# Optimization experiments

Hardware: AMD Instinct MI355X
Metric: run time of the kernel (lower is better)

## Reference

```python
import math
import jax, jax.numpy as jnp
import numpy as np

BH, S, DK = 64, 1024, 64   # batch*heads, seq_len, head dim
FG, FL = 32, 32            # global / local enrichment feature dims
H, B = 16, 4               # mask layout [heads, batch, seq]


def setup_inputs() -> dict:
    key = jax.random.key(0)
    k1, k2, k3, k4, k5, k6 = jax.random.split(key, 6)
    return {
        "query": jax.random.normal(k1, (BH, S, DK), dtype=jnp.float32),
        "key": jax.random.normal(k2, (BH, S, DK), dtype=jnp.float32),
        "value": jax.random.normal(k3, (BH, S, DK), dtype=jnp.float32),
        "local_f": jax.random.normal(k4, (BH, S, FL), dtype=jnp.float32),
        "global_f": jax.random.normal(k5, (BH, S, FG), dtype=jnp.float32),
        "mask": jax.random.randint(k6, (H, B, S), 0, 2, dtype=jnp.int32),
    }


def reference(query, key, value, local_f, global_f, mask):
    dk = query.shape[-1]
    # enrich q/k with global then local features (matches torch concat order)
    pq = jnp.concatenate([query, global_f, local_f], axis=2)   # [BH, S, dk+fg+fl]
    pk = jnp.concatenate([key, global_f, local_f], axis=2)
    scores = jnp.einsum("bqd,bkd->bqk", pq, pk) / math.sqrt(dk)  # [BH, S, S]
    # mask [H, B, S] -> [H*B, S] -> broadcast over query positions
    m = mask.reshape(-1, mask.shape[-1])[:, None, :]            # [H*B, 1, S]
    scores = jnp.where(m == 1, jnp.float32(-1e9), scores)
    attn = jax.nn.softmax(scores, axis=-1)
    return jnp.einsum("bqk,bkd->bqd", attn, value)              # [BH, S, dk]
```

## Files before the change

### kernel.cpp

```cpp
#include <hip/hip_runtime.h>
#include <hip/hip_bf16.h>


#define BHn 64
#define Sn  1024
#define NT  16
#define BK  64
#define BQ  64
#define KSTR 152
#define VSTR 72
#define KTILE (BK*KSTR*2)
#define VTILE (64*VSTR*2)
#define OSTR 68

typedef __attribute__((ext_vector_type(8)))  __bf16 bf16x8;
typedef __attribute__((ext_vector_type(16))) float  f32x16;
typedef __attribute__((ext_vector_type(4)))  unsigned int u32x4;
typedef __attribute__((ext_vector_type(2)))  unsigned int u32x2;

__device__ __forceinline__ unsigned f2bf1(float a){
    union { float f; unsigned u; } c; c.f = a;
    return (c.u + 0x7fffu + ((c.u >> 16) & 1u)) >> 16;
}
__device__ __forceinline__ unsigned f2bf2(float a, float b){
    return f2bf1(a) | (f2bf1(b) << 16);
}
__device__ __forceinline__ void wr4(unsigned short* p, float4 f){
    u32x2 w; w.x = f2bf2(f.x, f.y); w.y = f2bf2(f.z, f.w);
    *(u32x2*)p = w;
}
__device__ __forceinline__ unsigned pkbf(float a, float b){
    return __builtin_amdgcn_perm(__builtin_bit_cast(unsigned, b),
                                 __builtin_bit_cast(unsigned, a), 0x07060302u);
}
__device__ __forceinline__ void gld_lds16(const void* g, void* l){
    __builtin_amdgcn_global_load_lds(
        (const __attribute__((address_space(1))) unsigned int*)g,
        (__attribute__((address_space(3))) unsigned int*)l, 16, 0, 0);
}

__global__ __launch_bounds__(256)
void attn_prep(const float* __restrict__ K, const float* __restrict__ V,
               const float* __restrict__ LF, const float* __restrict__ GF,
               const int* __restrict__ M,
               unsigned short* __restrict__ Kp, unsigned short* __restrict__ Vp)
{
    __shared__ float vlds[64*65];
    const int tid = threadIdx.x;
    const int bh = blockIdx.x >> 4, ti = blockIdx.x & 15;
    const int kb = ti * BK;
    unsigned short* ktg = Kp + (size_t)(bh*NT + ti) * (BK*KSTR);
    unsigned int*   vtg = (unsigned int*)(Vp + (size_t)(bh*NT + ti) * (64*VSTR));

    #pragma unroll
    for (int i=0;i<4;i++){
        int idx = tid + 256*i, k = idx>>4, c = idx&15;
        float4 f = *(const float4*)(V + ((size_t)bh*Sn + kb + k)*64 + c*4);
        vlds[(c*4+0)*65 + k] = f.x;
        vlds[(c*4+1)*65 + k] = f.y;
        vlds[(c*4+2)*65 + k] = f.z;
        vlds[(c*4+3)*65 + k] = f.w;
    }
    #pragma unroll
    for (int i=0;i<4;i++){
        int idx = tid + 256*i, row = idx>>4, c = idx&15;
        float4 f = *(const float4*)(K + ((size_t)bh*Sn + kb + row)*64 + c*4);
        wr4(ktg + row*KSTR + c*4, f);
    }
    #pragma unroll
    for (int i=0;i<2;i++){
        int idx = tid + 256*i, row = idx>>3, c = idx&7;
        float4 f = *(const float4*)(GF + ((size_t)bh*Sn + kb + row)*32 + c*4);
        wr4(ktg + row*KSTR + 64 + c*4, f);
    }
    #pragma unroll
    for (int i=0;i<2;i++){
        int idx = tid + 256*i, row = idx>>3, c = idx&7;
        float4 f = *(const float4*)(LF + ((size_t)bh*Sn + kb + row)*32 + c*4);
        wr4(ktg + row*KSTR + 96 + c*4, f);
    }
    if (tid < BK){
        int mv = M[(size_t)bh*Sn + kb + tid];
        u32x4 w; w[0] = (mv == 1) ? 0x0000ceacu : 0u;
        w[1]=0u; w[2]=0u; w[3]=0u;
        *(u32x4*)(ktg + tid*KSTR + 128) = w;
        u32x4 z; z[0]=0u; z[1]=0u; z[2]=0u; z[3]=0u;
        *(u32x4*)(ktg + tid*KSTR + 136) = z;
        *(u32x4*)(ktg + tid*KSTR + 144) = z;
    }
    __syncthreads();
    #pragma unroll
    for (int i=0;i<8;i++){
        int idx = tid + 256*i, d = idx>>5, j = idx&31;
        vtg[d*36 + j] = f2bf2(vlds[d*65 + 2*j], vlds[d*65 + 2*j + 1]);
    }
}

__global__ __launch_bounds__(256, 4)
void attn_main(const float* __restrict__ Q, const unsigned short* __restrict__ Kp,
               const unsigned short* __restrict__ Vp,
               const float* __restrict__ GF, const float* __restrict__ LF,
               float* __restrict__ O)
{
    __shared__ __align__(16) unsigned char smem[KTILE + VTILE];
    unsigned short* kt_s = (unsigned short*)smem;
    unsigned short* vt_s = (unsigned short*)(smem + KTILE);

    const int tid  = threadIdx.x;
    const int wave = tid >> 6, lane = tid & 63;
    const int l31  = lane & 31, h = lane >> 5;
    const int qh   = wave >> 1;
    const int kp   = wave & 1;
    const int bh = blockIdx.x & 63;
    const int qb = blockIdx.x >> 6;
    const float SCL = 0.18033688011112042f;

    const int qrow = qb*BQ + qh*32 + l31;
    u32x4 qf[9];
    #pragma unroll
    for (int dc = 0; dc < 8; dc++){
        const int cb = dc*16 + 8*h;
        const float* src;
        if (cb < 64)      src = Q  + ((size_t)bh*Sn + qrow)*64 + cb;
        else if (cb < 96) src = GF + ((size_t)bh*Sn + qrow)*32 + (cb - 64);
        else              src = LF + ((size_t)bh*Sn + qrow)*32 + (cb - 96);
        float4 f0 = *(const float4*)src;
        float4 f1 = *(const float4*)(src + 4);
        qf[dc][0] = f2bf2(f0.x*SCL, f0.y*SCL);
        qf[dc][1] = f2bf2(f0.z*SCL, f0.w*SCL);
        qf[dc][2] = f2bf2(f1.x*SCL, f1.y*SCL);
        qf[dc][3] = f2bf2(f1.z*SCL, f1.w*SCL);
    }
    qf[8][0] = h ? 0u : 0x00003f80u;
    qf[8][1] = 0u; qf[8][2] = 0u; qf[8][3] = 0u;

    f32x16 oacc[2];
    #pragma unroll
    for (int dt=0; dt<2; dt++)
        #pragma unroll
        for (int r=0; r<16; r++) oacc[dt][r] = 0.f;
    float lrun = 0.f;

    for (int t = 0; t < NT; t++){
        __syncthreads();
        const unsigned char* gK = (const unsigned char*)Kp + (size_t)(bh*NT + t)*KTILE;
        const unsigned char* gV = (const unsigned char*)Vp + (size_t)(bh*NT + t)*VTILE;
        #pragma unroll
        for (int i=0;i<7;i++){
            int c = wave*7 + i;
            if (c < 19) gld_lds16(gK + (size_t)c*1024 + lane*16, smem + c*1024);
            else        gld_lds16(gV + (size_t)(c-19)*1024 + lane*16,
                                  smem + KTILE + (size_t)(c-19)*1024);
        }
        __syncthreads();

        f32x16 acc;
        #pragma unroll
        for (int r=0;r<16;r++) acc[r] = 0.f;
        #pragma unroll
        for (int dc=0; dc<9; dc++){
            u32x4 ar = *(const u32x4*)(kt_s + (kp*32 + l31)*KSTR + dc*16 + 8*h);
            acc = __builtin_amdgcn_mfma_f32_32x32x16_bf16(
                    __builtin_bit_cast(bf16x8, ar),
                    __builtin_bit_cast(bf16x8, qf[dc]), acc, 0, 0, 0);
        }

        float rs = 0.f;
        #pragma unroll
        for (int r=0;r<16;r++){
            float p = __builtin_amdgcn_exp2f(acc[r]);
            acc[r] = p; rs += p;
        }
        lrun += rs;

        unsigned pk[8], px[8];
        #pragma unroll
        for (int i=0;i<8;i++) pk[i] = pkbf(acc[2*i], acc[2*i+1]);
        #pragma unroll
        for (int i=0;i<8;i++) px[i] = (unsigned)__shfl_xor((int)pk[i], 32, 64);
        u32x4 b0, b1;
        b0[0] = h ? px[2] : pk[0];  b0[1] = h ? px[3] : pk[1];
        b0[2] = h ? pk[2] : px[0];  b0[3] = h ? pk[3] : px[1];
        b1[0] = h ? px[6] : pk[4];  b1[1] = h ? px[7] : pk[5];
        b1[2] = h ? pk[6] : px[4];  b1[3] = h ? pk[7] : px[5];

        #pragma unroll
        for (int dt=0;dt<2;dt++){
            u32x4 va0 = *(const u32x4*)(vt_s + (dt*32 + l31)*VSTR + kp*32 + 8*h);
            u32x4 va1 = *(const u32x4*)(vt_s + (dt*32 + l31)*VSTR + kp*32 + 16 + 8*h);
            oacc[dt] = __builtin_amdgcn_mfma_f32_32x32x16_bf16(
                    __builtin_bit_cast(bf16x8, va0),
                    __builtin_bit_cast(bf16x8, b0), oacc[dt], 0, 0, 0);
            oacc[dt] = __builtin_amdgcn_mfma_f32_32x32x16_bf16(
                    __builtin_bit_cast(bf16x8, va1),
                    __builtin_bit_cast(bf16x8, b1), oacc[dt], 0, 0, 0);
        }
    }

    __syncthreads();
    float lw = lrun + __shfl_xor(lrun, 32, 64);
    float* s1 = (float*)smem;
    float* s2 = (float*)(smem + 64*OSTR*4);
    if (kp == 1){
        #pragma unroll
        for (int dt=0;dt<2;dt++)
            #pragma unroll
            for (int rg=0;rg<4;rg++){
                float4 w;
                w.x = oacc[dt][rg*4+0]; w.y = oacc[dt][rg*4+1];
                w.z = oacc[dt][rg*4+2]; w.w = oacc[dt][rg*4+3];
                *(float4*)(s1 + (qh*32 + l31)*OSTR + dt*32 + rg*8 + 4*h) = w;
            }
        if (h == 0) s2[qh*32 + l31] = lw;
    }
    __syncthreads();
    if (kp == 0){
        float inv = 1.0f / (lw + s2[qh*32 + l31]);
        #pragma unroll
        for (int dt=0;dt<2;dt++)
            #pragma unroll
            for (int rg=0;rg<4;rg++){
                float* p = s1 + (qh*32 + l31)*OSTR + dt*32 + rg*8 + 4*h;
                float4 w = *(float4*)p;
                w.x = (w.x + oacc[dt][rg*4+0])*inv;
                w.y = (w.y + oacc[dt][rg*4+1])*inv;
                w.z = (w.z + oacc[dt][rg*4+2])*inv;
                w.w = (w.w + oacc[dt][rg*4+3])*inv;
                *(float4*)p = w;
            }
    }
    __syncthreads();
    #pragma unroll
    for (int i=0;i<4;i++){
        int idx = tid + 256*i, r = idx>>4, c = idx&15;
        *(float4*)(O + ((size_t)bh*Sn + qb*BQ + r)*64 + c*4) =
            *(const float4*)(s1 + r*OSTR + c*4);
    }
}

extern "C" void kernel_launch(void* const* d_in, const int* in_sizes, int n_in,
                              void* d_out, int out_size, void* d_ws, size_t ws_size,
                              hipStream_t stream) {
    const float* Q  = (const float*)d_in[0];
    const float* K  = (const float*)d_in[1];
    const float* V  = (const float*)d_in[2];
    const float* LF = (const float*)d_in[3];
    const float* GF = (const float*)d_in[4];
    const int*   M  = (const int*)d_in[5];
    float* O = (float*)d_out;

    unsigned short* Kp = (unsigned short*)d_ws;
    unsigned short* Vp = Kp + (size_t)BHn*NT*BK*KSTR;

    attn_prep<<<dim3(BHn*NT), dim3(256), 0, stream>>>(K, V, LF, GF, M, Kp, Vp);
    attn_main<<<dim3(BHn*NT), dim3(256), 0, stream>>>(Q, Kp, Vp, GF, LF, O);
}
```

Measured before the change: 159.3 us.

## Enlarge query tile to 128 rows, pre-permute V layout to drop lane shuffles

Result: faster. 148.7 us (-6.6%).

```diff
diff --git a/kernel.cpp b/kernel.cpp
--- a/kernel.cpp
+++ b/kernel.cpp
@@ -5,18 +5,16 @@
 #define BHn 64
 #define Sn  1024
 #define NT  16
-#define BK  64
-#define BQ  64
-#define KSTR 152
+#define KSTR 144
 #define VSTR 72
-#define KTILE (BK*KSTR*2)
+#define KTILE (64*KSTR*2)
 #define VTILE (64*VSTR*2)
 #define OSTR 68
+#define SMEMB (128*OSTR*4 + 512)
 
 typedef __attribute__((ext_vector_type(8)))  __bf16 bf16x8;
 typedef __attribute__((ext_vector_type(16))) float  f32x16;
 typedef __attribute__((ext_vector_type(4)))  unsigned int u32x4;
-typedef __attribute__((ext_vector_type(2)))  unsigned int u32x2;
 
 __device__ __forceinline__ unsigned f2bf1(float a){
     union { float f; unsigned u; } c; c.f = a;
@@ -24,10 +22,6 @@
 }
 __device__ __forceinline__ unsigned f2bf2(float a, float b){
     return f2bf1(a) | (f2bf1(b) << 16);
-}
-__device__ __forceinline__ void wr4(unsigned short* p, float4 f){
-    u32x2 w; w.x = f2bf2(f.x, f.y); w.y = f2bf2(f.z, f.w);
-    *(u32x2*)p = w;
 }
 __device__ __forceinline__ unsigned pkbf(float a, float b){
     return __builtin_amdgcn_perm(__builtin_bit_cast(unsigned, b),
@@ -45,64 +39,67 @@
                const int* __restrict__ M,
                unsigned short* __restrict__ Kp, unsigned short* __restrict__ Vp)
 {
-    __shared__ float vlds[64*65];
     const int tid = threadIdx.x;
-    const int bh = blockIdx.x >> 4, ti = blockIdx.x & 15;
-    const int kb = ti * BK;
-    unsigned short* ktg = Kp + (size_t)(bh*NT + ti) * (BK*KSTR);
+    const int bh = blockIdx.x >> 4, ti = blockIdx.x & 15, kb = ti*64;
+    unsigned short* ktg = Kp + (size_t)(bh*NT + ti) * (64*KSTR);
     unsigned int*   vtg = (unsigned int*)(Vp + (size_t)(bh*NT + ti) * (64*VSTR));
 
-    #pragma unroll
-    for (int i=0;i<4;i++){
-        int idx = tid + 256*i, k = idx>>4, c = idx&15;
-        float4 f = *(const float4*)(V + ((size_t)bh*Sn + kb + k)*64 + c*4);
-        vlds[(c*4+0)*65 + k] = f.x;
-        vlds[(c*4+1)*65 + k] = f.y;
-        vlds[(c*4+2)*65 + k] = f.z;
-        vlds[(c*4+3)*65 + k] = f.w;
-    }
-    #pragma unroll
-    for (int i=0;i<4;i++){
-        int idx = tid + 256*i, row = idx>>4, c = idx&15;
-        float4 f = *(const float4*)(K + ((size_t)bh*Sn + kb + row)*64 + c*4);
-        wr4(ktg + row*KSTR + c*4, f);
-    }
     #pragma unroll
     for (int i=0;i<2;i++){
         int idx = tid + 256*i, row = idx>>3, c = idx&7;
-        float4 f = *(const float4*)(GF + ((size_t)bh*Sn + kb + row)*32 + c*4);
-        wr4(ktg + row*KSTR + 64 + c*4, f);
-    }
-    #pragma unroll
-    for (int i=0;i<2;i++){
-        int idx = tid + 256*i, row = idx>>3, c = idx&7;
-        float4 f = *(const float4*)(LF + ((size_t)bh*Sn + kb + row)*32 + c*4);
-        wr4(ktg + row*KSTR + 96 + c*4, f);
-    }
-    if (tid < BK){
+        const float* s = K + ((size_t)bh*Sn + kb + row)*64 + c*8;
+        float4 f0 = *(const float4*)s, f1 = *(const float4*)(s+4);
+        u32x4 w; w[0]=f2bf2(f0.x,f0.y); w[1]=f2bf2(f0.z,f0.w);
+        w[2]=f2bf2(f1.x,f1.y); w[3]=f2bf2(f1.z,f1.w);
+        *(u32x4*)(ktg + row*KSTR + c*8) = w;
+    }
+    {
+        int row = tid>>2, c = tid&3;
+        const float* s = GF + ((size_t)bh*Sn + kb + row)*32 + c*8;
+        float4 f0 = *(const float4*)s, f1 = *(const float4*)(s+4);
+        u32x4 w; w[0]=f2bf2(f0.x,f0.y); w[1]=f2bf2(f0.z,f0.w);
+        w[2]=f2bf2(f1.x,f1.y); w[3]=f2bf2(f1.z,f1.w);
+        *(u32x4*)(ktg + row*KSTR + 64 + c*8) = w;
+    }
+    {
+        int row = tid>>2, c = tid&3;
+        const float* s = LF + ((size_t)bh*Sn + kb + row)*32 + c*8;
+        float4 f0 = *(const float4*)s, f1 = *(const float4*)(s+4);
+        u32x4 w; w[0]=f2bf2(f0.x,f0.y); w[1]=f2bf2(f0.z,f0.w);
+        w[2]=f2bf2(f1.x,f1.y); w[3]=f2bf2(f1.z,f1.w);
+        *(u32x4*)(ktg + row*KSTR + 96 + c*8) = w;
+    }
+    if (tid < 64){
         int mv = M[(size_t)bh*Sn + kb + tid];
         u32x4 w; w[0] = (mv == 1) ? 0x0000ceacu : 0u;
         w[1]=0u; w[2]=0u; w[3]=0u;
         *(u32x4*)(ktg + tid*KSTR + 128) = w;
         u32x4 z; z[0]=0u; z[1]=0u; z[2]=0u; z[3]=0u;
         *(u32x4*)(ktg + tid*KSTR + 136) = z;
-        *(u32x4*)(ktg + tid*KSTR + 144) = z;
-    }
-    __syncthreads();
-    #pragma unroll
-    for (int i=0;i<8;i++){
-        int idx = tid + 256*i, d = idx>>5, j = idx&31;
-        vtg[d*36 + j] = f2bf2(vlds[d*65 + 2*j], vlds[d*65 + 2*j + 1]);
-    }
-}
-
-__global__ __launch_bounds__(256, 4)
+    }
+    {
+        int d = tid & 63, g = tid >> 6;
+        const float* vb = V + ((size_t)bh*Sn + kb + 16*g)*64 + d;
+        const int pm[16] = {0,1,2,3, 8,9,10,11, 4,5,6,7, 12,13,14,15};
+        unsigned w[8];
+        #pragma unroll
+        for (int m=0;m<8;m++)
+            w[m] = f2bf2(vb[(size_t)pm[2*m]*64], vb[(size_t)pm[2*m+1]*64]);
+        u32x4 a, b;
+        a[0]=w[0]; a[1]=w[1]; a[2]=w[2]; a[3]=w[3];
+        b[0]=w[4]; b[1]=w[5]; b[2]=w[6]; b[3]=w[7];
+        *(u32x4*)(vtg + d*36 + g*8)     = a;
+        *(u32x4*)(vtg + d*36 + g*8 + 4) = b;
+    }
+}
+
+__global__ __launch_bounds__(512, 4)
 void attn_main(const float* __restrict__ Q, const unsigned short* __restrict__ Kp,
                const unsigned short* __restrict__ Vp,
                const float* __restrict__ GF, const float* __restrict__ LF,
                float* __restrict__ O)
 {
-    __shared__ __align__(16) unsigned char smem[KTILE + VTILE];
+    __shared__ __align__(16) unsigned char smem[SMEMB];
     unsigned short* kt_s = (unsigned short*)smem;
     unsigned short* vt_s = (unsigned short*)(smem + KTILE);
 
@@ -115,7 +112,7 @@
     const int qb = blockIdx.x >> 6;
     const float SCL = 0.18033688011112042f;
 
-    const int qrow = qb*BQ + qh*32 + l31;
+    const int qrow = qb*128 + qh*32 + l31;
     u32x4 qf[9];
     #pragma unroll
     for (int dc = 0; dc < 8; dc++){
@@ -146,11 +143,11 @@
         const unsigned char* gK = (const unsigned char*)Kp + (size_t)(bh*NT + t)*KTILE;
         const unsigned char* gV = (const unsigned char*)Vp + (size_t)(bh*NT + t)*VTILE;
         #pragma unroll
-        for (int i=0;i<7;i++){
-            int c = wave*7 + i;
-            if (c < 19) gld_lds16(gK + (size_t)c*1024 + lane*16, smem + c*1024);
-            else        gld_lds16(gV + (size_t)(c-19)*1024 + lane*16,
-                                  smem + KTILE + (size_t)(c-19)*1024);
+        for (int i=0;i<4;i++){
+            int c = wave + 8*i;
+            if (c < 18)      gld_lds16(gK + (size_t)c*1024 + lane*16, smem + c*1024);
+            else if (c < 27) gld_lds16(gV + (size_t)(c-18)*1024 + lane*16,
+                                       smem + KTILE + (size_t)(c-18)*1024);
         }
         __syncthreads();
 
@@ -173,16 +170,12 @@
         }
         lrun += rs;
 
-        unsigned pk[8], px[8];
+        unsigned pk[8];
         #pragma unroll
         for (int i=0;i<8;i++) pk[i] = pkbf(acc[2*i], acc[2*i+1]);
-        #pragma unroll
-        for (int i=0;i<8;i++) px[i] = (unsigned)__shfl_xor((int)pk[i], 32, 64);
         u32x4 b0, b1;
-        b0[0] = h ? px[2] : pk[0];  b0[1] = h ? px[3] : pk[1];
-        b0[2] = h ? pk[2] : px[0];  b0[3] = h ? pk[3] : px[1];
-        b1[0] = h ? px[6] : pk[4];  b1[1] = h ? px[7] : pk[5];
-        b1[2] = h ? pk[6] : px[4];  b1[3] = h ? pk[7] : px[5];
+        b0[0]=pk[0]; b0[1]=pk[1]; b0[2]=pk[2]; b0[3]=pk[3];
+        b1[0]=pk[4]; b1[1]=pk[5]; b1[2]=pk[6]; b1[3]=pk[7];
 
         #pragma unroll
         for (int dt=0;dt<2;dt++){
@@ -200,7 +193,7 @@
     __syncthreads();
     float lw = lrun + __shfl_xor(lrun, 32, 64);
     float* s1 = (float*)smem;
-    float* s2 = (float*)(smem + 64*OSTR*4);
+    float* s2 = (float*)(smem + 128*OSTR*4);
     if (kp == 1){
         #pragma unroll
         for (int dt=0;dt<2;dt++)
@@ -232,8 +225,8 @@
     __syncthreads();
     #pragma unroll
     for (int i=0;i<4;i++){
-        int idx = tid + 256*i, r = idx>>4, c = idx&15;
-        *(float4*)(O + ((size_t)bh*Sn + qb*BQ + r)*64 + c*4) =
+        int idx = tid + 512*i, r = idx>>4, c = idx&15;
+        *(float4*)(O + ((size_t)bh*Sn + qb*128 + r)*64 + c*4) =
             *(const float4*)(s1 + r*OSTR + c*4);
     }
 }
@@ -250,8 +243,8 @@
     float* O = (float*)d_out;
 
     unsigned short* Kp = (unsigned short*)d_ws;
-    unsigned short* Vp = Kp + (size_t)BHn*NT*BK*KSTR;
+    unsigned short* Vp = Kp + (size_t)BHn*NT*64*KSTR;
 
     attn_prep<<<dim3(BHn*NT), dim3(256), 0, stream>>>(K, V, LF, GF, M, Kp, Vp);
-    attn_main<<<dim3(BHn*NT), dim3(256), 0, stream>>>(Q, Kp, Vp, GF, LF, O);
-}
+    attn_main<<<dim3(BHn*(Sn/128)), dim3(512), 0, stream>>>(Q, Kp, Vp, GF, LF, O);
+}
```
